# Kernel tuning notes

Measured on AMD Instinct MI355X. Metric: run time of the kernel, lower is better.

Reference implementation:

```python
import math
import jax, jax.numpy as jnp
import numpy as np

D_MODEL = 1024
N_POLES = 32        # d_state // 2
DIRECTIONS = 2      # bidirectional
SEQ_LEN = 4096
DT_MIN, DT_MAX = 1e-3, 1e-1


def setup_inputs() -> dict:
    key = jax.random.key(0)
    k_dt, k_c = jax.random.split(key, 2)
    # log_dt ~ U[log(dt_min), log(dt_max)]
    log_dt = jax.random.uniform(k_dt, (D_MODEL,), dtype=jnp.float32) \
        * (math.log(DT_MAX) - math.log(DT_MIN)) + math.log(DT_MIN)
    # S4D-Lin initialization: real part -0.5, imag part pi*n
    log_a_real = jnp.log(0.5 * jnp.ones((D_MODEL, N_POLES), dtype=jnp.float32))
    a_imag = math.pi * jnp.tile(jnp.arange(N_POLES, dtype=jnp.float32)[None, :], (D_MODEL, 1))
    # complex coeffs stored as real view [..., 2]
    coeffs = jax.random.normal(k_c, (DIRECTIONS, D_MODEL, N_POLES, 2), dtype=jnp.float32)
    return {
        "log_dt": log_dt,
        "log_a_real": log_a_real,
        "a_imag": a_imag,
        "coeffs": coeffs,
        "sequence_length": SEQ_LEN,
    }


def reference(log_dt, log_a_real, a_imag, coeffs, sequence_length):
    dt = jnp.exp(log_dt)                                   # [H]
    c = coeffs[..., 0] + 1j * coeffs[..., 1]               # [dir, H, N] complex
    a = -jnp.exp(log_a_real) + 1j * a_imag                 # [H, N] complex
    timeline = jnp.arange(sequence_length, dtype=jnp.float32)  # [L]
    delta_a = a * dt[:, None]                              # [H, N]
    # Vandermonde matrix exp(delta_a * l): [H, N, L] complex (the big intermediate)
    vand = jnp.exp(delta_a[:, :, None] * timeline)
    scaled_c = c * (jnp.exp(delta_a) - 1.0) / a            # [dir, H, N]
    # contract over poles N -> [dir, H, L]
    kernels = 2.0 * jnp.real(jnp.einsum('dhn,hnl->dhl', scaled_c, vand))
    return kernels
```

## Files before the change

kernel.cpp:

```cpp
#include <hip/hip_runtime.h>
#include <math.h>


typedef float v2f __attribute__((ext_vector_type(2)));

constexpr int H     = 1024;
constexpr int NP    = 32;
constexpr int L     = 4096;
constexpr int BLOCK = 256;
constexpr int CHUNK = 16;

constexpr float  TWOPI    = 6.283185307179586f;
constexpr double INV2PI_D = 0.15915494309189535;

__global__ __launch_bounds__(BLOCK, 4)
void ssm_vand_kernel(const float* __restrict__ log_dt,
                     const float* __restrict__ log_a_real,
                     const float* __restrict__ a_imag,
                     const float* __restrict__ coeffs,
                     float* __restrict__ out)
{
    const int h = blockIdx.x;
    const int t = threadIdx.x;

    __shared__ float4 pole[NP * 3];

    if (t < NP) {
        const int n = t;
        const float dtf = expf(log_dt[h]);
        const float ar  = -expf(log_a_real[h * NP + n]);
        const float ai  = a_imag[h * NP + n];
        const float dar = ar * dtf;
        const float dai = ai * dtf;

        const double rate  = (double)ai * (double)dtf * INV2PI_D;
        const float  rhi   = (float)(rate - floor(rate));

        const float e256 = expf(256.0f * dar);
        double r256 = 256.0 * rate;
        r256 -= floor(r256);
        float s256, c256;
        sincosf((float)r256 * TWOPI, &s256, &c256);
        const float zr = e256 * c256;
        const float zi = e256 * s256;

        const float ed = expf(dar);
        float sd, cd;
        sincosf(dai, &sd, &cd);
        const float emr = ed * cd - 1.0f;
        const float emi = ed * sd;
        const float inv = 1.0f / (ar * ar + ai * ai);
        const float gr  = (emr * ar + emi * ai) * inv;
        const float gi  = (emi * ar - emr * ai) * inv;

        const float cr0 = coeffs[((0 * H + h) * NP + n) * 2 + 0];
        const float ci0 = coeffs[((0 * H + h) * NP + n) * 2 + 1];
        const float cr1 = coeffs[((1 * H + h) * NP + n) * 2 + 0];
        const float ci1 = coeffs[((1 * H + h) * NP + n) * 2 + 1];

        pole[n * 3 + 0] = make_float4(dar, rhi, zr, zi);
        pole[n * 3 + 1] = make_float4(2.0f * zr,
                                      zr * zr + zi * zi,
                                      2.0f * (cr0 * gr - ci0 * gi),
                                      2.0f * (cr0 * gi + ci0 * gr));
        pole[n * 3 + 2] = make_float4(2.0f * (cr1 * gr - ci1 * gi),
                                      2.0f * (cr1 * gi + ci1 * gr),
                                      0.0f, 0.0f);
    }
    __syncthreads();

    v2f acc[CHUNK];
    #pragma unroll
    for (int j = 0; j < CHUNK; ++j) acc[j] = (v2f){0.0f, 0.0f};

    const float lf = (float)t;

    #pragma unroll 1
    for (int n = 0; n < NP; ++n) {
        const float4 pa = pole[n * 3 + 0];
        const float4 pb = pole[n * 3 + 1];
        const float4 pc = pole[n * 3 + 2];

        const float m = __expf(pa.x * lf);
        const float ph = pa.y * lf;
        const float rev = ph - floorf(ph);
        float s, c;
        __sincosf(rev * TWOPI, &s, &c);
        const float wr = m * c;
        const float wi = m * s;
        const float wr2 = fmaf(wr, pa.z, -(wi * pa.w));
        const float wi2 = fmaf(wi, pa.z,  (wr * pa.w));

        const v2f sr = {pb.z, pc.x};
        const v2f si = {pb.w, pc.y};
        const v2f p  = {pb.x, pb.x};
        const v2f q  = {pb.y, pb.y};

        v2f xp = __builtin_elementwise_fma(sr, (v2f){wr,  wr},  -(si * (v2f){wi,  wi}));
        v2f x  = __builtin_elementwise_fma(sr, (v2f){wr2, wr2}, -(si * (v2f){wi2, wi2}));

        acc[0] += xp;
        acc[1] += x;

        #pragma unroll
        for (int j = 2; j < CHUNK; ++j) {
            const v2f nx = __builtin_elementwise_fma(p, x, -(q * xp));
            acc[j] += nx;
            xp = x;
            x  = nx;
        }
    }

    float* o0 = out + (size_t)h * L + t;
    float* o1 = o0 + (size_t)H * L;
    #pragma unroll
    for (int j = 0; j < CHUNK; ++j) {
        o0[j * BLOCK] = acc[j].x;
        o1[j * BLOCK] = acc[j].y;
    }
}

extern "C" void kernel_launch(void* const* d_in, const int* in_sizes, int n_in,
                              void* d_out, int out_size, void* d_ws, size_t ws_size,
                              hipStream_t stream) {
    const float* log_dt     = (const float*)d_in[0];
    const float* log_a_real = (const float*)d_in[1];
    const float* a_imag     = (const float*)d_in[2];
    const float* coeffs     = (const float*)d_in[3];
    float* out = (float*)d_out;

    ssm_vand_kernel<<<dim3(H), dim3(BLOCK), 0, stream>>>(
        log_dt, log_a_real, a_imag, coeffs, out);
}
```

Measured before the change: 89.55 us.

## Lengthen per-thread recurrence chunk and prefetch next pole parameters from LDS

Halves the block to 128 threads while doubling each thread's output chunk to 32, so each thread extends the Chebyshev-style recurrence across more timesteps per pole. The pole rotation factor is recomputed for a stride of 128. Pole parameters for the next iteration are loaded from shared memory ahead of use. The aim is to amortize the per-pole exp/sincos cost over more outputs, at the price of more register pressure, lower occupancy and longer recurrence error accumulation.

```diff
diff --git a/kernel.cpp b/kernel.cpp
--- a/kernel.cpp
+++ b/kernel.cpp
@@ -7,13 +7,13 @@
 constexpr int H     = 1024;
 constexpr int NP    = 32;
 constexpr int L     = 4096;
-constexpr int BLOCK = 256;
-constexpr int CHUNK = 16;
+constexpr int BLOCK = 128;
+constexpr int CHUNK = 32;
 
 constexpr float  TWOPI    = 6.283185307179586f;
 constexpr double INV2PI_D = 0.15915494309189535;
 
-__global__ __launch_bounds__(BLOCK, 4)
+__global__ __launch_bounds__(BLOCK, 2)
 void ssm_vand_kernel(const float* __restrict__ log_dt,
                      const float* __restrict__ log_a_real,
                      const float* __restrict__ a_imag,
@@ -36,13 +36,13 @@
         const double rate  = (double)ai * (double)dtf * INV2PI_D;
         const float  rhi   = (float)(rate - floor(rate));
 
-        const float e256 = expf(256.0f * dar);
-        double r256 = 256.0 * rate;
-        r256 -= floor(r256);
-        float s256, c256;
-        sincosf((float)r256 * TWOPI, &s256, &c256);
-        const float zr = e256 * c256;
-        const float zi = e256 * s256;
+        const float e128 = expf(128.0f * dar);
+        double r128 = 128.0 * rate;
+        r128 -= floor(r128);
+        float s128, c128;
+        sincosf((float)r128 * TWOPI, &s128, &c128);
+        const float zr = e128 * c128;
+        const float zi = e128 * s128;
 
         const float ed = expf(dar);
         float sd, cd;
@@ -75,19 +75,24 @@
 
     const float lf = (float)t;
 
+    float4 pa = pole[0];
+    float4 pb = pole[1];
+    float4 pc = pole[2];
+
     #pragma unroll 1
     for (int n = 0; n < NP; ++n) {
-        const float4 pa = pole[n * 3 + 0];
-        const float4 pb = pole[n * 3 + 1];
-        const float4 pc = pole[n * 3 + 2];
+        const int np1 = (n + 1 < NP) ? (n + 1) : n;
+        const float4 qa = pole[np1 * 3 + 0];
+        const float4 qb = pole[np1 * 3 + 1];
+        const float4 qc = pole[np1 * 3 + 2];
 
-        const float m = __expf(pa.x * lf);
+        const float mg = __expf(pa.x * lf);
         const float ph = pa.y * lf;
         const float rev = ph - floorf(ph);
         float s, c;
         __sincosf(rev * TWOPI, &s, &c);
-        const float wr = m * c;
-        const float wi = m * s;
+        const float wr = mg * c;
+        const float wi = mg * s;
         const float wr2 = fmaf(wr, pa.z, -(wi * pa.w));
         const float wi2 = fmaf(wi, pa.z,  (wr * pa.w));
 
@@ -109,6 +114,8 @@
             xp = x;
             x  = nx;
         }
+
+        pa = qa; pb = qb; pc = qc;
     }
 
     float* o0 = out + (size_t)h * L + t;
```

Result: no change. 89.97 us (+0.5%).
